# Performance work log

Measured on AMD Instinct MI355X. Metric: run time of the kernel, lower is better.

## Reference

```python
import jax, jax.numpy as jnp
import numpy as np

B, N, D = 2, 2048, 256
H = 8
HD = D // H
SCALE = HD ** 0.5  # NOTE: source MULTIPLIES by sqrt(head_dim)
EPS = 1e-5
DFF = 4 * D


def setup_inputs() -> dict:
    key = jax.random.key(0)
    ks = jax.random.split(key, 9)
    s = lambda fan_in: 1.0 / np.sqrt(fan_in)
    return {
        "x": jax.random.normal(ks[0], (B, N, D), dtype=jnp.float32),
        # weights stored [in, out] (transposed torch Linear)
        "qkv_w": jax.random.normal(ks[1], (D, 3 * D), dtype=jnp.float32) * s(D),
        "proj_w": jax.random.normal(ks[2], (D, D), dtype=jnp.float32) * s(D),
        "proj_b": jax.random.normal(ks[3], (D,), dtype=jnp.float32) * 0.01,
        "fc1_w": jax.random.normal(ks[4], (D, DFF), dtype=jnp.float32) * s(D),
        "fc1_b": jax.random.normal(ks[5], (DFF,), dtype=jnp.float32) * 0.01,
        "fc2_w": jax.random.normal(ks[6], (DFF, D), dtype=jnp.float32) * s(DFF),
        "fc2_b": jax.random.normal(ks[7], (D,), dtype=jnp.float32) * 0.01,
        "ln1_g": jnp.ones((D,), dtype=jnp.float32),
        "ln1_b": jnp.zeros((D,), dtype=jnp.float32),
    }


def _layernorm(x, g, b):
    mu = jnp.mean(x, axis=-1, keepdims=True)
    var = jnp.mean(jnp.square(x - mu), axis=-1, keepdims=True)
    return (x - mu) * jax.lax.rsqrt(var + EPS) * g + b


def reference(x, qkv_w, proj_w, proj_b, fc1_w, fc1_b, fc2_w, fc2_b, ln1_g, ln1_b):
    b, n, d = x.shape
    # --- MHA ---
    qkv = (x @ qkv_w).reshape(b, n, 3, H, HD)
    q = qkv[:, :, 0].transpose(0, 2, 1, 3)  # [B,H,N,HD]
    k = qkv[:, :, 1].transpose(0, 2, 1, 3)
    v = qkv[:, :, 2].transpose(0, 2, 1, 3)
    att = jnp.einsum("bhqd,bhkd->bhqk", q, k) * SCALE  # multiplied, per source
    att = jax.nn.softmax(att, axis=-1)
    out = jnp.einsum("bhqk,bhkd->bhqd", att, v)
    out = out.transpose(0, 2, 1, 3).reshape(b, n, d)
    out = out @ proj_w + proj_b
    # --- post-norm residual ---
    net = _layernorm(out + x, ln1_g, ln1_b)
    shortcut = net
    # --- MLP (NO activation in source forward) ---
    net = (net @ fc1_w + fc1_b) @ fc2_w + fc2_b
    return net + shortcut
```

## Files before the change

kernel.cpp:

```cpp
#include <hip/hip_runtime.h>


typedef __attribute__((ext_vector_type(8))) short short8;
typedef __attribute__((ext_vector_type(4))) short short4v;
typedef __attribute__((ext_vector_type(8))) _Float16 half8;
typedef __attribute__((ext_vector_type(4))) _Float16 half4;
typedef __attribute__((ext_vector_type(2))) __fp16 fp16x2;
typedef __attribute__((ext_vector_type(4))) float floatx4;
typedef __attribute__((ext_vector_type(2))) unsigned int uint2v;
typedef unsigned short u16;

#define MFMAG(a,b,c)  __builtin_amdgcn_mfma_f32_16x16x32_f16((a),(b),(c),0,0,0)
#if __has_builtin(__builtin_amdgcn_mfma_f32_16x16x16_f16)
#define MFMAPV(a,b,c) __builtin_amdgcn_mfma_f32_16x16x16_f16((a),(b),(c),0,0,0)
#else
#define MFMAPV(a,b,c) __builtin_amdgcn_mfma_f32_16x16x16f16((a),(b),(c),0,0,0)
#endif
#define CLF 8.1615404f

#if __has_builtin(__builtin_amdgcn_exp2f)
#define EX2(x) __builtin_amdgcn_exp2f(x)
#else
#define EX2(x) exp2f(x)
#endif

__device__ __forceinline__ float bf2f(u16 u) { return __uint_as_float(((unsigned)u) << 16); }
__device__ __forceinline__ float h2f(u16 u) { _Float16 h = *(_Float16*)&u; return (float)h; }
__device__ __forceinline__ u16 f2h(float f) { _Float16 h = (_Float16)f; return *(u16*)&h; }
__device__ __forceinline__ unsigned pkh2(float a, float b) {
#if __has_builtin(__builtin_amdgcn_cvt_pkrtz)
  fp16x2 h = __builtin_amdgcn_cvt_pkrtz(a, b);
  return *(unsigned*)&h;
#else
  return (unsigned)f2h(a) | ((unsigned)f2h(b) << 16);
#endif
}
__device__ __forceinline__ void gll16(const void* g, void* l) {
  __builtin_amdgcn_global_load_lds((const __attribute__((address_space(1))) void*)g,
                                   (__attribute__((address_space(3))) void*)l, 16, 0, 0);
}

__global__ __launch_bounds__(256) void prep_k(
    const void* __restrict__ x, const void* __restrict__ qkv_w,
    const void* __restrict__ proj_w, const void* __restrict__ fc1_w,
    const void* __restrict__ fc2_w, const void* __restrict__ proj_b,
    const void* __restrict__ fc1_b, const void* __restrict__ fc2_b,
    const void* __restrict__ ln_g, const void* __restrict__ ln_b,
    u16* __restrict__ x_f, u16* __restrict__ wq_f,
    u16* __restrict__ wt_proj, u16* __restrict__ wt_fc1, u16* __restrict__ wt_fc2,
    u16* __restrict__ b_proj, u16* __restrict__ b_fc1, u16* __restrict__ b_fc2,
    u16* __restrict__ g_ln, u16* __restrict__ bb_ln)
{
  __shared__ u16 tr[64][70];
  const int lane = threadIdx.x & 63;
  const float probe = bf2f(((const u16*)qkv_w)[lane]);
  const bool f32 = __ballot(!(fabsf(probe) < 1000.0f)) != 0ull;
  const int bid = blockIdx.x, tid = threadIdx.x;
  #define RD(p, i) (f32 ? ((const float*)(p))[i] : bf2f(((const u16*)(p))[i]))
  if (bid < 1024) {
    const size_t i = (size_t)bid * 1024 + tid * 4;
    const u16 o0 = f2h(RD(x, i)),     o1 = f2h(RD(x, i + 1));
    const u16 o2 = f2h(RD(x, i + 2)), o3 = f2h(RD(x, i + 3));
    short4v sv = {(short)o0, (short)o1, (short)o2, (short)o3};
    *(short4v*)&x_f[i] = sv;
  } else if (bid < 1216) {
    int idx = bid - 1024;
    const void* src; u16* dst; int Ns, Kt, tk, tn;
    if (idx < 48)       { src = qkv_w;  dst = wq_f;    Ns = 768;  Kt = 256;
                          tk = idx & 3;  tn = idx >> 2; }
    else if (idx < 64)  { idx -= 48;  src = proj_w; dst = wt_proj; Ns = 256; Kt = 256;
                          tk = idx & 3;  tn = idx >> 2; }
    else if (idx < 128) { idx -= 64;  src = fc1_w;  dst = wt_fc1;  Ns = 1024; Kt = 256;
                          tk = idx & 3;  tn = idx >> 2; }
    else                { idx -= 128; src = fc2_w;  dst = wt_fc2;  Ns = 256;  Kt = 1024;
                          tk = idx & 15; tn = idx >> 4; }
    const int k0 = tk * 64, n0 = tn * 64;
    const int r = tid >> 6, c = tid & 63;
#pragma unroll
    for (int p = 0; p < 16; ++p) {
      const int k = k0 + p * 4 + r;
      tr[c][p * 4 + r] = f2h(RD(src, (size_t)k * Ns + n0 + c));
    }
    __syncthreads();
#pragma unroll
    for (int p = 0; p < 16; ++p) {
      const int n = n0 + p * 4 + r;
      dst[(size_t)n * Kt + k0 + c] = tr[p * 4 + r][c];
    }
  } else {
    const int j = (bid - 1216) * 256 + tid;
    if (j < 256)       b_proj[j]        = f2h(RD(proj_b, j));
    else if (j < 1280) b_fc1[j - 256]   = f2h(RD(fc1_b, j - 256));
    else if (j < 1536) b_fc2[j - 1280]  = f2h(RD(fc2_b, j - 1280));
    else if (j < 1792) g_ln[j - 1536]   = f2h(RD(ln_g, j - 1536));
    else if (j < 2048) bb_ln[j - 1792]  = f2h(RD(ln_b, j - 1792));
  }
  #undef RD
}

template<int TW, int EPI, bool BIAS, bool RES, bool COMB>
__global__ __launch_bounds__(256) void gemm_k(
    const u16* __restrict__ A, const u16* __restrict__ Bt, const u16* __restrict__ A2,
    const u16* __restrict__ bias, const u16* __restrict__ res,
    void* __restrict__ out0, u16* __restrict__ aux1, u16* __restrict__ aux3,
    const float* __restrict__ muc,
    int M, int Nn, int K)
{
  constexpr int BT = TW * 32;
  constexpr int NC = TW / 2;
  __shared__ __align__(16) u16 As[BT][40];
  __shared__ __align__(16) u16 Bs[BT][40];
  __shared__ __align__(16) u16 Vt[(EPI == 2) ? 64 * 72 : 1];
  const int tid = threadIdx.x;
  const int m0 = blockIdx.y * BT, n0 = blockIdx.x * BT;
  const int wid = tid >> 6, lane = tid & 63;
  const int wm = (wid >> 1) * (TW * 16), wn = (wid & 1) * (TW * 16);
  const int lm = lane & 15, quad = lane >> 4;

  floatx4 zero = {0.f, 0.f, 0.f, 0.f};
  floatx4 acc[TW][TW];
#pragma unroll
  for (int i = 0; i < TW; ++i)
#pragma unroll
    for (int j = 0; j < TW; ++j) acc[i][j] = zero;

  auto comb8 = [&](int t, int col8) -> short8 {
    const size_t o = (size_t)t * 256 + col8;
    const int h = col8 >> 5;
    const float m0_ = muc[t * 8 + h],          m1_ = muc[32768 + t * 8 + h];
    const float m2_ = muc[65536 + t * 8 + h],  m3_ = muc[98304 + t * 8 + h];
    const float M = fmaxf(fmaxf(m0_, m1_), fmaxf(m2_, m3_));
    float w0 = EX2(m0_ - M), w1 = EX2(m1_ - M), w2 = EX2(m2_ - M), w3 = EX2(m3_ - M);
    const float inv = 1.f / (w0 + w1 + w2 + w3);
    w0 *= inv; w1 *= inv; w2 *= inv; w3 *= inv;
    short8 a0 = *(const short8*)&A[o],  a1 = *(const short8*)&A[o + 1048576];
    short8 a2 = *(const short8*)&A2[o], a3 = *(const short8*)&A2[o + 1048576];
    float v[8];
#pragma unroll
    for (int j = 0; j < 8; ++j)
      v[j] = w0 * h2f((u16)a0[j]) + w1 * h2f((u16)a1[j])
           + w2 * h2f((u16)a2[j]) + w3 * h2f((u16)a3[j]);
    uint2v uu0 = {pkh2(v[0], v[1]), pkh2(v[2], v[3])};
    uint2v uu1 = {pkh2(v[4], v[5]), pkh2(v[6], v[7])};
    short8 r;
    *(uint2v*)&r = uu0; *((uint2v*)&r + 1) = uu1;
    return r;
  };

  int srow[NC], soff[NC];
#pragma unroll
  for (int c = 0; c < NC; ++c) {
    const int cid = tid * NC + c;
    srow[c] = cid >> 2; soff[c] = (cid & 3) * 8;
  }

  short8 ra0[NC], rb0[NC];
  auto ld = [&](int kk) {
#pragma unroll
    for (int c = 0; c < NC; ++c) {
      rb0[c] = *(const short8*)&Bt[(size_t)(n0 + srow[c]) * K + kk + soff[c]];
      if (COMB) ra0[c] = comb8(m0 + srow[c], kk + soff[c]);
      else      ra0[c] = *(const short8*)&A[(size_t)(m0 + srow[c]) * K + kk + soff[c]];
    }
  };
  ld(0);
  for (int k0 = 0; k0 < K; k0 += 32) {
    if (k0) __syncthreads();
#pragma unroll
    for (int c = 0; c < NC; ++c) {
      *(short8*)&As[srow[c]][soff[c]] = ra0[c];
      *(short8*)&Bs[srow[c]][soff[c]] = rb0[c];
    }
    __syncthreads();
    if (k0 + 32 < K) ld(k0 + 32);
    half8 fa[TW], fb[TW];
#pragma unroll
    for (int t = 0; t < TW; ++t) {
      fa[t] = *(const half8*)&As[wm + t * 16 + lm][quad * 8];
      fb[t] = *(const half8*)&Bs[wn + t * 16 + lm][quad * 8];
    }
#pragma unroll
    for (int i = 0; i < TW; ++i)
#pragma unroll
      for (int j = 0; j < TW; ++j)
        acc[i][j] = MFMAG(fa[i], fb[j], acc[i][j]);
  }

  if (EPI == 2 && n0 >= 512) {
    __syncthreads();
#pragma unroll
    for (int i = 0; i < TW; ++i)
#pragma unroll
      for (int j = 0; j < TW; ++j)
#pragma unroll
        for (int r = 0; r < 4; ++r)
          Vt[(wn + j * 16 + lm) * 72 + wm + i * 16 + quad * 4 + r] = f2h(acc[i][j][r]);
    __syncthreads();
    const int bb = m0 >> 11, n = m0 & 2047;
#pragma unroll
    for (int pass = 0; pass < 2; ++pass) {
      const int dl = (tid >> 3) + pass * 32;
      const int oct = tid & 7;
      const int col = n0 - 512 + dl;
      const int d = col & 31, hh = col >> 5;
      short8 v = *(const short8*)&Vt[dl * 72 + oct * 8];
      *(short8*)&((u16*)out0)[(size_t)((bb * 8 + hh) * 32 + d) * 2048 + n + oct * 8] = v;
    }
    return;
  }

#pragma unroll
  for (int i = 0; i < TW; ++i) {
    const int rowb = m0 + wm + i * 16 + quad * 4;
#pragma unroll
    for (int j = 0; j < TW; ++j) {
      const int col = n0 + wn + j * 16 + lm;
      const float bv = BIAS ? h2f(bias[col]) : 0.f;
#pragma unroll
      for (int r = 0; r < 4; ++r) {
        const int row = rowb + r;
        float v = acc[i][j][r] + bv;
        const size_t o = (size_t)row * Nn + col;
        if (RES) v += h2f(res[o]);
        if (EPI == 0) {
          ((float*)out0)[o] = v;
        } else if (EPI == 1) {
          ((u16*)out0)[o] = f2h(v);
        } else {
          if (col < 256) aux1[(size_t)row * 256 + col] = f2h(v);
          else           aux3[(size_t)row * 256 + (col - 256)] = f2h(v);
        }
      }
    }
  }
}

__global__ __launch_bounds__(512) void gemm8_k(
    const u16* __restrict__ A, const u16* __restrict__ Bt,
    const u16* __restrict__ bias, const u16* __restrict__ res,
    float* __restrict__ out0, int Nn, int K)
{
  __shared__ __align__(16) u16 As[64][40];
  __shared__ __align__(16) u16 Bs[64][40];
  const int tid = threadIdx.x;
  const int m0 = blockIdx.y * 64, n0 = blockIdx.x * 64;
  const int wid = tid >> 6, lane = tid & 63;
  const int wm = (wid & 3) * 16, wn = (wid >> 2) * 32;
  const int lm = lane & 15, quad = lane >> 4;

  floatx4 zero = {0.f, 0.f, 0.f, 0.f};
  floatx4 acc0 = zero, acc1 = zero;

  const int sgrp = tid >> 8, stid = tid & 255;
  const int srow = stid >> 2, soff = (stid & 3) * 8;
  const u16* sp = sgrp ? Bt : A;
  const int sbase = sgrp ? n0 : m0;

  short8 rr;
  rr = *(const short8*)&sp[(size_t)(sbase + srow) * K + soff];
  for (int k0 = 0; k0 < K; k0 += 32) {
    if (k0) __syncthreads();
    if (sgrp) *(short8*)&Bs[srow][soff] = rr;
    else      *(short8*)&As[srow][soff] = rr;
    __syncthreads();
    if (k0 + 32 < K)
      rr = *(const short8*)&sp[(size_t)(sbase + srow) * K + k0 + 32 + soff];
    half8 fa = *(const half8*)&As[wm + lm][quad * 8];
    half8 fb0 = *(const half8*)&Bs[wn + lm][quad * 8];
    half8 fb1 = *(const half8*)&Bs[wn + 16 + lm][quad * 8];
    acc0 = MFMAG(fa, fb0, acc0);
    acc1 = MFMAG(fa, fb1, acc1);
  }

  const int rowb = m0 + wm + quad * 4;
  const int col0 = n0 + wn + lm, col1 = col0 + 16;
  const float bv0 = h2f(bias[col0]), bv1 = h2f(bias[col1]);
#pragma unroll
  for (int r = 0; r < 4; ++r) {
    const int row = rowb + r;
    const size_t o0 = (size_t)row * Nn + col0;
    const size_t o1 = (size_t)row * Nn + col1;
    out0[o0] = acc0[r] + bv0 + h2f(res[o0]);
    out0[o1] = acc1[r] + bv1 + h2f(res[o1]);
  }
}

__global__ __launch_bounds__(512) void projln8_k(
    const u16* __restrict__ A,
    const u16* __restrict__ A2,
    const u16* __restrict__ Bt,
    const u16* __restrict__ bias,
    const u16* xh,
    const u16* __restrict__ g, const u16* __restrict__ bb,
    const float* __restrict__ muc,
    u16* net)
{
  __shared__ __align__(16) u16 As[16][40];
  __shared__ __align__(16) u16 Bs[256][40];
  __shared__ float ss[8][16], ssq[8][16];
  const int tid = threadIdx.x;
  const int m0 = blockIdx.x * 16;
  const int wid = tid >> 6, lane = tid & 63;
  const int lm = lane & 15, quad = lane >> 4;

  floatx4 zero = {0.f, 0.f, 0.f, 0.f};
  floatx4 acc0 = zero, acc1 = zero;

  auto comb8 = [&](int t, int col8) -> short8 {
    const size_t o = (size_t)t * 256 + col8;
    const int h = col8 >> 5;
    const float m0_ = muc[t * 8 + h],          m1_ = muc[32768 + t * 8 + h];
    const float m2_ = muc[65536 + t * 8 + h],  m3_ = muc[98304 + t * 8 + h];
    const float M = fmaxf(fmaxf(m0_, m1_), fmaxf(m2_, m3_));
    float w0 = EX2(m0_ - M), w1 = EX2(m1_ - M), w2 = EX2(m2_ - M), w3 = EX2(m3_ - M);
    const float inv = 1.f / (w0 + w1 + w2 + w3);
    w0 *= inv; w1 *= inv; w2 *= inv; w3 *= inv;
    short8 a0 = *(const short8*)&A[o],  a1 = *(const short8*)&A[o + 1048576];
    short8 a2 = *(const short8*)&A2[o], a3 = *(const short8*)&A2[o + 1048576];
    float v[8];
#pragma unroll
    for (int j = 0; j < 8; ++j)
      v[j] = w0 * h2f((u16)a0[j]) + w1 * h2f((u16)a1[j])
           + w2 * h2f((u16)a2[j]) + w3 * h2f((u16)a3[j]);
    uint2v uu0 = {pkh2(v[0], v[1]), pkh2(v[2], v[3])};
    uint2v uu1 = {pkh2(v[4], v[5]), pkh2(v[6], v[7])};
    short8 r;
    *(uint2v*)&r = uu0; *((uint2v*)&r + 1) = uu1;
    return r;
  };

  const int arow = lane >> 2, aoff = (lane & 3) * 8;
  int brow0 = wid * 32 + (lane >> 2), brow1 = brow0 + 16;
  const int boff = (lane & 3) * 8;

  short8 ra, rb0, rb1;
  if (wid == 0) ra = comb8(m0 + arow, aoff);
  rb0 = *(const short8*)&Bt[(size_t)brow0 * 256 + boff];
  rb1 = *(const short8*)&Bt[(size_t)brow1 * 256 + boff];

  for (int k0 = 0; k0 < 256; k0 += 32) {
    if (k0) __syncthreads();
    if (wid == 0) *(short8*)&As[arow][aoff] = ra;
    *(short8*)&Bs[brow0][boff] = rb0;
    *(short8*)&Bs[brow1][boff] = rb1;
    __syncthreads();
    if (k0 + 32 < 256) {
      if (wid == 0) ra = comb8(m0 + arow, k0 + 32 + aoff);
      rb0 = *(const short8*)&Bt[(size_t)brow0 * 256 + k0 + 32 + boff];
      rb1 = *(const short8*)&Bt[(size_t)brow1 * 256 + k0 + 32 + boff];
    }
    half8 fa = *(const half8*)&As[lm][quad * 8];
    half8 fb0 = *(const half8*)&Bs[wid * 32 + lm][quad * 8];
    half8 fb1 = *(const half8*)&Bs[wid * 32 + 16 + lm][quad * 8];
    acc0 = MFMAG(fa, fb0, acc0);
    acc1 = MFMAG(fa, fb1, acc1);
  }

  const int col0 = wid * 32 + lm, col1 = col0 + 16;
  const float bv0 = h2f(bias[col0]), bv1 = h2f(bias[col1]);
  float s[4], sq[4], v0[4], v1[4];
#pragma unroll
  for (int r = 0; r < 4; ++r) {
    const int row = quad * 4 + r;
    const float a = acc0[r] + bv0 + h2f(xh[(size_t)(m0 + row) * 256 + col0]);
    const float b = acc1[r] + bv1 + h2f(xh[(size_t)(m0 + row) * 256 + col1]);
    v0[r] = a; v1[r] = b;
    s[r] = a + b; sq[r] = a * a + b * b;
  }
#pragma unroll
  for (int d = 1; d < 16; d <<= 1)
#pragma unroll
    for (int r = 0; r < 4; ++r) {
      s[r] += __shfl_xor(s[r], d);
      sq[r] += __shfl_xor(sq[r], d);
    }
  if (lm == 0)
#pragma unroll
    for (int r = 0; r < 4; ++r) { ss[wid][quad * 4 + r] = s[r]; ssq[wid][quad * 4 + r] = sq[r]; }
  __syncthreads();
#pragma unroll
  for (int r = 0; r < 4; ++r) {
    const int row = quad * 4 + r;
    float ts = 0.f, tq = 0.f;
#pragma unroll
    for (int w = 0; w < 8; ++w) { ts += ss[w][row]; tq += ssq[w][row]; }
    const float mean = ts * (1.f / 256.f);
    const float var = tq * (1.f / 256.f) - mean * mean;
    const float is = rsqrtf(var + 1e-5f);
    net[(size_t)(m0 + row) * 256 + col0] =
        f2h((v0[r] - mean) * is * h2f(g[col0]) + h2f(bb[col0]));
    net[(size_t)(m0 + row) * 256 + col1] =
        f2h((v1[r] - mean) * is * h2f(g[col1]) + h2f(bb[col1]));
  }
}

template<int CHUNKS>
__global__ __launch_bounds__(256) void attn_k(
    const u16* __restrict__ qf16, const u16* __restrict__ kf16,
    const u16* __restrict__ vt, u16* __restrict__ outp, u16* __restrict__ out23,
    float* __restrict__ mu)
{
  __shared__ __align__(16) u16 Ks[2][64][32];
  __shared__ __align__(16) u16 Vs[2][32][64];
  const int tid = threadIdx.x, wid = tid >> 6, lane = tid & 63;
  const int lm = lane & 15, quad = lane >> 4;
  const int bid = blockIdx.x;
  const int chunk = (CHUNKS > 1) ? (bid >> 9) : 0;
  const int qblk = bid & 31, bh = (bid >> 5) & 15;
  const int b = bh >> 3, h = bh & 7;
  const int q0 = qblk * 64 + wid * 16;
  const size_t tb = (size_t)b * 2048;
  const int NT = 32 / CHUNKS;
  const int kofs = chunk * (2048 / CHUNKS);

  half8 qh;
  { size_t off = (tb + q0 + lm) * 256 + h * 32 + quad * 8;
    qh = *(const half8*)&qf16[off]; }

  const int kkey = tid >> 2, kg = tid & 3;
  const size_t kb = (tb + kofs + kkey) * 256 + h * 32 + kg * 8;
  const int vd = tid >> 3, vp = tid & 7, vk8 = vp ^ (vd & 7);
  const size_t vb = (size_t)(bh * 32 + vd) * 2048 + kofs + vk8 * 8;

  gll16(kf16 + kb, (u16*)Ks + tid * 8);
  gll16(vt  + vb,  (u16*)Vs + tid * 8);

  float mrun = -1e30f, lrun = 0.f;
  floatx4 o0 = {0.f,0.f,0.f,0.f}, o1 = {0.f,0.f,0.f,0.f};

  for (int kt = 0; kt < NT; ++kt) {
    const int buf = kt & 1;
    __syncthreads();
    if (kt < NT - 1) {
      const int nb = (buf ^ 1) * 2048;
      const size_t ko = (size_t)(kt + 1) * 16384;
      const size_t vo = (size_t)(kt + 1) * 64;
      gll16(kf16 + kb + ko, (u16*)Ks + nb + tid * 8);
      gll16(vt  + vb + vo,  (u16*)Vs + nb + tid * 8);
    }

    floatx4 z[4];
#pragma unroll
    for (int kf = 0; kf < 4; ++kf) {
      half8 khf = *(const half8*)&Ks[buf][kf * 16 + lm][quad * 8];
      floatx4 zz = {0.f,0.f,0.f,0.f};
      z[kf] = MFMAG(khf, qh, zz);
    }
    float zm = fmaxf(fmaxf(fmaxf(z[0][0], z[0][1]), fmaxf(z[0][2], z[0][3])),
               fmaxf(fmaxf(z[1][0], z[1][1]), fmaxf(z[1][2], z[1][3])));
    zm = fmaxf(zm, fmaxf(fmaxf(fmaxf(z[2][0], z[2][1]), fmaxf(z[2][2], z[2][3])),
                   fmaxf(fmaxf(z[3][0], z[3][1]), fmaxf(z[3][2], z[3][3]))));
    zm = fmaxf(zm, __shfl_xor(zm, 16));
    zm = fmaxf(zm, __shfl_xor(zm, 32));
    const float mn = fmaxf(mrun, zm);
    const float alpha = EX2((mrun - mn) * CLF);
    const float mc = mn * CLF;
    mrun = mn;
    float ls = 0.f;
    half4 pb[4];
#pragma unroll
    for (int kf = 0; kf < 4; ++kf) {
      const float p0 = EX2(__builtin_fmaf(z[kf][0], CLF, -mc));
      const float p1 = EX2(__builtin_fmaf(z[kf][1], CLF, -mc));
      const float p2 = EX2(__builtin_fmaf(z[kf][2], CLF, -mc));
      const float p3 = EX2(__builtin_fmaf(z[kf][3], CLF, -mc));
      ls += (p0 + p1) + (p2 + p3);
      uint2v uu = {pkh2(p0, p1), pkh2(p2, p3)};
      pb[kf] = *(half4*)&uu;
    }
    ls += __shfl_xor(ls, 16);
    ls += __shfl_xor(ls, 32);
    lrun = lrun * alpha + ls;
#pragma unroll
    for (int r = 0; r < 4; ++r) { o0[r] *= alpha; o1[r] *= alpha; }
    const u16* vbase = (const u16*)Vs + buf * 2048;
#pragma unroll
    for (int kf = 0; kf < 4; ++kf) {
      const int k8 = 2 * kf + (quad >> 1);
      const int d0 = lm, d1 = 16 + lm;
      half4 vf0 = *(const half4*)(vbase + (d0 * 8 + (k8 ^ (d0 & 7))) * 8 + (quad & 1) * 4);
      half4 vf1 = *(const half4*)(vbase + (d1 * 8 + (k8 ^ (d1 & 7))) * 8 + (quad & 1) * 4);
      o0 = MFMAPV(vf0, pb[kf], o0);
      o1 = MFMAPV(vf1, pb[kf], o1);
    }
  }
  const float inv = 1.0f / lrun;
  const size_t tok = tb + q0 + lm;
  u16* dst = ((CHUNKS > 2 && chunk >= 2) ? out23 : outp) + (size_t)(chunk & 1) * 1048576;
  const size_t rowo = tok * 256 + h * 32;
#pragma unroll
  for (int r = 0; r < 4; ++r) {
    dst[rowo + quad * 4 + r]      = f2h(o0[r] * inv);
    dst[rowo + 16 + quad * 4 + r] = f2h(o1[r] * inv);
  }
  if (CHUNKS > 1 && quad == 0)
    mu[chunk * 32768 + tok * 8 + h] = __builtin_fmaf(mrun, CLF, __log2f(lrun));
}

template<int CHUNKS>
__global__ __launch_bounds__(256) void combine_k(u16* __restrict__ d,
                                                 const u16* __restrict__ e,
                                                 const float* __restrict__ mu)
{
  const int t = blockIdx.x, c = threadIdx.x, h = c >> 5;
  const size_t o = (size_t)t * 256 + c;
  float m[CHUNKS];
  float M = -1e30f;
#pragma unroll
  for (int i = 0; i < CHUNKS; ++i) { m[i] = mu[i * 32768 + t * 8 + h]; M = fmaxf(M, m[i]); }
  float wsum = 0.f, acc = 0.f;
#pragma unroll
  for (int i = 0; i < CHUNKS; ++i) {
    const float w = EX2(m[i] - M);
    const u16 v = (i < 2) ? d[o + (size_t)i * 1048576] : e[o + (size_t)(i - 2) * 1048576];
    wsum += w; acc += w * h2f(v);
  }
  d[o] = f2h(acc / wsum);
}

__global__ __launch_bounds__(256) void ln_k(const float* __restrict__ pf,
                                            const u16* __restrict__ xh,
                                            const u16* __restrict__ g,
                                            const u16* __restrict__ bta,
                                            u16* __restrict__ net)
{
  const int t = blockIdx.x, c = threadIdx.x;
  const size_t o = (size_t)t * 256 + c;
  float v = pf[o] + h2f(xh[o]);
  float s = v, s2 = v * v;
#pragma unroll
  for (int d = 1; d < 64; d <<= 1) { s += __shfl_xor(s, d); s2 += __shfl_xor(s2, d); }
  __shared__ float ss[4], ss2[4];
  const int w = c >> 6;
  if ((c & 63) == 0) { ss[w] = s; ss2[w] = s2; }
  __syncthreads();
  s = ss[0] + ss[1] + ss[2] + ss[3];
  s2 = ss2[0] + ss2[1] + ss2[2] + ss2[3];
  const float mu = s * (1.f / 256.f);
  const float var = s2 * (1.f / 256.f) - mu * mu;
  const float is = rsqrtf(var + 1e-5f);
  net[o] = f2h((v - mu) * is * h2f(g[c]) + h2f(bta[c]));
}

extern "C" void kernel_launch(void* const* d_in, const int* in_sizes, int n_in,
                              void* d_out, int out_size, void* d_ws, size_t ws_size,
                              hipStream_t stream) {
  const void* x      = d_in[0];
  const void* qkv_w  = d_in[1];
  const void* proj_w = d_in[2];
  const void* proj_b = d_in[3];
  const void* fc1_w  = d_in[4];
  const void* fc1_b  = d_in[5];
  const void* fc2_w  = d_in[6];
  const void* fc2_b  = d_in[7];
  const void* ln_g   = d_in[8];
  const void* ln_b   = d_in[9];

  char* ws = (char*)d_ws;
  u16* b_proj  = (u16*)(ws + 4096);
  u16* b_fc1   = (u16*)(ws + 8192);
  u16* b_fc2   = (u16*)(ws + 12288);
  u16* g_ln    = (u16*)(ws + 16384);
  u16* bb_ln   = (u16*)(ws + 20480);
  u16* wq_f    = (u16*)(ws + 131072);
  u16* wt_proj = (u16*)(ws + 524288);
  u16* wt_fc1  = (u16*)(ws + 655360);
  u16* wt_fc2  = (u16*)(ws + 1179648);
  u16* x_f     = (u16*)(ws + 2097152);
  u16* q_f16   = (u16*)(ws + 4194304);
  u16* k_f16   = (u16*)(ws + 6291456);
  u16* vt      = (u16*)(ws + 8388608);
  float* mu    = (float*)(ws + 10485760);
  u16* out23   = (u16*)(ws + 11010048);
  u16* attn    = (u16*)d_out;

  u16* net4    = x_f;
  u16* hbuf4   = (u16*)(ws + 4194304);

  float* projf = (float*)(ws + 4194304);
  u16* net     = (u16*)(ws + 11010048);
  u16* hbuf    = (u16*)(ws + 2097152);

  const bool sk4 = ws_size >= 15204352;
  const bool sk2 = ws_size >= 11010048;

  prep_k<<<1224, 256, 0, stream>>>(x, qkv_w, proj_w, fc1_w, fc2_w,
                                   proj_b, fc1_b, fc2_b, ln_g, ln_b,
                                   x_f, wq_f, wt_proj, wt_fc1, wt_fc2,
                                   b_proj, b_fc1, b_fc2, g_ln, bb_ln);

  gemm_k<2, 2, false, false, false><<<dim3(12, 64), 256, 0, stream>>>(
      x_f, wq_f, nullptr, nullptr, nullptr, vt, q_f16, k_f16, nullptr, 4096, 768, 256);
  if (sk4) {
    attn_k<4><<<2048, 256, 0, stream>>>(q_f16, k_f16, vt, attn, out23, mu);
    projln8_k<<<256, 512, 0, stream>>>(attn, out23, wt_proj, b_proj, x_f,
                                       g_ln, bb_ln, mu, net4);
    gemm_k<2, 1, true, false, false><<<dim3(16, 64), 256, 0, stream>>>(
        net4, wt_fc1, nullptr, b_fc1, nullptr, hbuf4, nullptr, nullptr, nullptr,
        4096, 1024, 256);
    gemm8_k<<<dim3(4, 64), 512, 0, stream>>>(
        hbuf4, wt_fc2, b_fc2, net4, (float*)d_out, 256, 1024);
    return;
  }
  if (sk2) {
    attn_k<2><<<1024, 256, 0, stream>>>(q_f16, k_f16, vt, attn, nullptr, mu);
    combine_k<2><<<4096, 256, 0, stream>>>(attn, nullptr, mu);
    gemm_k<2, 0, true, false, false><<<dim3(4, 64), 256, 0, stream>>>(
        attn, wt_proj, nullptr, b_proj, nullptr, projf, nullptr, nullptr, nullptr,
        4096, 256, 256);
  } else {
    attn_k<1><<<512, 256, 0, stream>>>(q_f16, k_f16, vt, attn, nullptr, nullptr);
    gemm_k<2, 0, true, false, false><<<dim3(4, 64), 256, 0, stream>>>(
        attn, wt_proj, nullptr, b_proj, nullptr, projf, nullptr, nullptr, nullptr,
        4096, 256, 256);
  }
  ln_k<<<4096, 256, 0, stream>>>(projf, x_f, g_ln, bb_ln, net);
  gemm_k<2, 1, true, false, false><<<dim3(16, 64), 256, 0, stream>>>(
      net, wt_fc1, nullptr, b_fc1, nullptr, hbuf, nullptr, nullptr, nullptr,
      4096, 1024, 256);
  gemm_k<2, 0, true, true, false><<<dim3(4, 64), 256, 0, stream>>>(
      hbuf, wt_fc2, nullptr, b_fc2, net, d_out, nullptr, nullptr, nullptr,
      4096, 256, 1024);
}
```

Baseline: 144.5 us.

## Fuse input/weight conversion into QKV GEMM kernel and read raw x in proj-LN

Adds a qkvprep_k kernel that loads raw x and qkv_w directly, converts them to fp16 on the fly and computes the QKV GEMM. Extra blocks in the same launch transpose and convert the remaining weights and biases. This removes the separate prep kernel launch and the round trip of writing and rereading converted x and qkv weights. projln8_k now reads the raw input for the residual, so x_f is no longer needed. The cost is strided, uncoalesced loads of qkv_w inside the GEMM and repeated conversion work in every block.

```diff
diff --git a/kernel.cpp b/kernel.cpp
--- a/kernel.cpp
+++ b/kernel.cpp
@@ -38,6 +38,159 @@
 __device__ __forceinline__ void gll16(const void* g, void* l) {
   __builtin_amdgcn_global_load_lds((const __attribute__((address_space(1))) void*)g,
                                    (__attribute__((address_space(3))) void*)l, 16, 0, 0);
+}
+
+__global__ __launch_bounds__(256) void qkvprep_k(
+    const void* __restrict__ x, const void* __restrict__ qkv_w,
+    const void* __restrict__ proj_w, const void* __restrict__ fc1_w,
+    const void* __restrict__ fc2_w, const void* __restrict__ proj_b,
+    const void* __restrict__ fc1_b, const void* __restrict__ fc2_b,
+    const void* __restrict__ ln_g, const void* __restrict__ ln_b,
+    u16* __restrict__ wt_proj, u16* __restrict__ wt_fc1, u16* __restrict__ wt_fc2,
+    u16* __restrict__ b_proj, u16* __restrict__ b_fc1, u16* __restrict__ b_fc2,
+    u16* __restrict__ g_ln, u16* __restrict__ bb_ln,
+    u16* __restrict__ vt, u16* __restrict__ qf, u16* __restrict__ kf)
+{
+  __shared__ __align__(16) u16 lds[9728];
+  const int tid = threadIdx.x;
+  const int lane = tid & 63;
+  const float probe = bf2f(((const u16*)qkv_w)[lane]);
+  const bool f32 = __ballot(!(fabsf(probe) < 1000.0f)) != 0ull;
+  const int bid = blockIdx.x;
+  #define RD(p, i) (f32 ? ((const float*)(p))[i] : bf2f(((const u16*)(p))[i]))
+
+  if (bid >= 768) {
+    int idx = bid - 768;
+    if (idx < 144) {
+      u16 (*tr)[70] = (u16(*)[70])lds;
+      const void* src; u16* dst; int Ns, Kt, tk, tn;
+      if (idx < 16)      { src = proj_w; dst = wt_proj; Ns = 256;  Kt = 256;
+                           tk = idx & 3;  tn = idx >> 2; }
+      else if (idx < 80) { idx -= 16; src = fc1_w; dst = wt_fc1; Ns = 1024; Kt = 256;
+                           tk = idx & 3;  tn = idx >> 2; }
+      else               { idx -= 80; src = fc2_w; dst = wt_fc2; Ns = 256;  Kt = 1024;
+                           tk = idx & 15; tn = idx >> 4; }
+      const int k0 = tk * 64, n0v = tn * 64;
+      const int r = tid >> 6, c = tid & 63;
+#pragma unroll
+      for (int p = 0; p < 16; ++p) {
+        const int k = k0 + p * 4 + r;
+        tr[c][p * 4 + r] = f2h(RD(src, (size_t)k * Ns + n0v + c));
+      }
+      __syncthreads();
+#pragma unroll
+      for (int p = 0; p < 16; ++p) {
+        const int n = n0v + p * 4 + r;
+        dst[(size_t)n * Kt + k0 + c] = tr[p * 4 + r][c];
+      }
+    } else {
+      const int j = (idx - 144) * 256 + tid;
+      if (j < 256)       b_proj[j]        = f2h(RD(proj_b, j));
+      else if (j < 1280) b_fc1[j - 256]   = f2h(RD(fc1_b, j - 256));
+      else if (j < 1536) b_fc2[j - 1280]  = f2h(RD(fc2_b, j - 1280));
+      else if (j < 1792) g_ln[j - 1536]   = f2h(RD(ln_g, j - 1536));
+      else if (j < 2048) bb_ln[j - 1792]  = f2h(RD(ln_b, j - 1792));
+    }
+    return;
+  }
+  #undef RD
+
+  u16 (*As)[40] = (u16(*)[40])lds;
+  u16 (*Bs)[40] = (u16(*)[40])(lds + 2560);
+  u16* Vt = lds + 5120;
+  const int mb = bid / 12, nb = bid % 12;
+  const int m0 = mb * 64, n0 = nb * 64;
+  const int wid = tid >> 6;
+  const int wm = (wid >> 1) * 32, wn = (wid & 1) * 32;
+  const int lm = lane & 15, quad = lane >> 4;
+
+  floatx4 zero = {0.f, 0.f, 0.f, 0.f};
+  floatx4 acc[2][2] = {{zero, zero}, {zero, zero}};
+
+  const int arow = tid >> 2, aoff = (tid & 3) * 8;
+  const int bn = tid & 63, bk8 = (tid >> 6) * 8;
+
+  short8 rah, rbh;
+  auto ld = [&](int kk) {
+    if (f32) {
+      const float* xp = (const float*)x + (size_t)(m0 + arow) * 256 + kk + aoff;
+      floatx4 a0 = *(const floatx4*)xp;
+      floatx4 a1 = *(const floatx4*)(xp + 4);
+#pragma unroll
+      for (int j = 0; j < 4; ++j) {
+        rah[j]     = (short)f2h(a0[j]);
+        rah[4 + j] = (short)f2h(a1[j]);
+      }
+      const float* wp = (const float*)qkv_w + (size_t)(kk + bk8) * 768 + n0 + bn;
+#pragma unroll
+      for (int j = 0; j < 8; ++j) rbh[j] = (short)f2h(wp[(size_t)j * 768]);
+    } else {
+      short8 a = *(const short8*)((const u16*)x + (size_t)(m0 + arow) * 256 + kk + aoff);
+#pragma unroll
+      for (int j = 0; j < 8; ++j) rah[j] = (short)f2h(bf2f((u16)a[j]));
+      const u16* wp = (const u16*)qkv_w + (size_t)(kk + bk8) * 768 + n0 + bn;
+#pragma unroll
+      for (int j = 0; j < 8; ++j) rbh[j] = (short)f2h(bf2f(wp[(size_t)j * 768]));
+    }
+  };
+  ld(0);
+  for (int k0 = 0; k0 < 256; k0 += 32) {
+    if (k0) __syncthreads();
+    *(short8*)&As[arow][aoff] = rah;
+    *(short8*)&Bs[bn][bk8] = rbh;
+    __syncthreads();
+    if (k0 + 32 < 256) ld(k0 + 32);
+    half8 fa[2], fb[2];
+#pragma unroll
+    for (int t = 0; t < 2; ++t) {
+      fa[t] = *(const half8*)&As[wm + t * 16 + lm][quad * 8];
+      fb[t] = *(const half8*)&Bs[wn + t * 16 + lm][quad * 8];
+    }
+#pragma unroll
+    for (int i = 0; i < 2; ++i)
+#pragma unroll
+      for (int j = 0; j < 2; ++j)
+        acc[i][j] = MFMAG(fa[i], fb[j], acc[i][j]);
+  }
+
+  if (n0 >= 512) {
+    __syncthreads();
+#pragma unroll
+    for (int i = 0; i < 2; ++i)
+#pragma unroll
+      for (int j = 0; j < 2; ++j)
+#pragma unroll
+        for (int r = 0; r < 4; ++r)
+          Vt[(wn + j * 16 + lm) * 72 + wm + i * 16 + quad * 4 + r] = f2h(acc[i][j][r]);
+    __syncthreads();
+    const int bb = m0 >> 11, n = m0 & 2047;
+#pragma unroll
+    for (int pass = 0; pass < 2; ++pass) {
+      const int dl = (tid >> 3) + pass * 32;
+      const int oct = tid & 7;
+      const int col = n0 - 512 + dl;
+      const int d = col & 31, hh = col >> 5;
+      short8 v = *(const short8*)&Vt[dl * 72 + oct * 8];
+      *(short8*)&vt[(size_t)((bb * 8 + hh) * 32 + d) * 2048 + n + oct * 8] = v;
+    }
+    return;
+  }
+
+#pragma unroll
+  for (int i = 0; i < 2; ++i) {
+    const int rowb = m0 + wm + i * 16 + quad * 4;
+#pragma unroll
+    for (int j = 0; j < 2; ++j) {
+      const int col = n0 + wn + j * 16 + lm;
+#pragma unroll
+      for (int r = 0; r < 4; ++r) {
+        const int row = rowb + r;
+        const u16 hv = f2h(acc[i][j][r]);
+        if (col < 256) qf[(size_t)row * 256 + col] = hv;
+        else           kf[(size_t)row * 256 + (col - 256)] = hv;
+      }
+    }
+  }
 }
 
 __global__ __launch_bounds__(256) void prep_k(
@@ -290,10 +443,11 @@
     const u16* __restrict__ A2,
     const u16* __restrict__ Bt,
     const u16* __restrict__ bias,
-    const u16* xh,
+    const void* __restrict__ xraw,
+    const void* __restrict__ probew,
     const u16* __restrict__ g, const u16* __restrict__ bb,
     const float* __restrict__ muc,
-    u16* net)
+    u16* __restrict__ net)
 {
   __shared__ __align__(16) u16 As[16][40];
   __shared__ __align__(16) u16 Bs[256][40];
@@ -302,6 +456,8 @@
   const int m0 = blockIdx.x * 16;
   const int wid = tid >> 6, lane = tid & 63;
   const int lm = lane & 15, quad = lane >> 4;
+  const float probe = bf2f(((const u16*)probew)[lane]);
+  const bool f32 = __ballot(!(fabsf(probe) < 1000.0f)) != 0ull;
 
   floatx4 zero = {0.f, 0.f, 0.f, 0.f};
   floatx4 acc0 = zero, acc1 = zero;
@@ -362,8 +518,12 @@
 #pragma unroll
   for (int r = 0; r < 4; ++r) {
     const int row = quad * 4 + r;
-    const float a = acc0[r] + bv0 + h2f(xh[(size_t)(m0 + row) * 256 + col0]);
-    const float b = acc1[r] + bv1 + h2f(xh[(size_t)(m0 + row) * 256 + col1]);
+    const size_t o0 = (size_t)(m0 + row) * 256 + col0;
+    const size_t o1 = (size_t)(m0 + row) * 256 + col1;
+    const float x0 = f32 ? ((const float*)xraw)[o0] : bf2f(((const u16*)xraw)[o0]);
+    const float x1 = f32 ? ((const float*)xraw)[o1] : bf2f(((const u16*)xraw)[o1]);
+    const float a = acc0[r] + bv0 + h2f(f2h(x0));
+    const float b = acc1[r] + bv1 + h2f(f2h(x1));
     v0[r] = a; v1[r] = b;
     s[r] = a + b; sq[r] = a * a + b * b;
   }
@@ -574,7 +734,7 @@
   u16* out23   = (u16*)(ws + 11010048);
   u16* attn    = (u16*)d_out;
 
-  u16* net4    = x_f;
+  u16* net4    = (u16*)(ws + 2097152);
   u16* hbuf4   = (u16*)(ws + 4194304);
 
   float* projf = (float*)(ws + 4194304);
@@ -584,16 +744,14 @@
   const bool sk4 = ws_size >= 15204352;
   const bool sk2 = ws_size >= 11010048;
 
-  prep_k<<<1224, 256, 0, stream>>>(x, qkv_w, proj_w, fc1_w, fc2_w,
-                                   proj_b, fc1_b, fc2_b, ln_g, ln_b,
-                                   x_f, wq_f, wt_proj, wt_fc1, wt_fc2,
-                                   b_proj, b_fc1, b_fc2, g_ln, bb_ln);
-
-  gemm_k<2, 2, false, false, false><<<dim3(12, 64), 256, 0, stream>>>(
-      x_f, wq_f, nullptr, nullptr, nullptr, vt, q_f16, k_f16, nullptr, 4096, 768, 256);
   if (sk4) {
+    qkvprep_k<<<920, 256, 0, stream>>>(x, qkv_w, proj_w, fc1_w, fc2_w,
+                                       proj_b, fc1_b, fc2_b, ln_g, ln_b,
+                                       wt_proj, wt_fc1, wt_fc2,
+                                       b_proj, b_fc1, b_fc2, g_ln, bb_ln,
+                                       vt, q_f16, k_f16);
     attn_k<4><<<2048, 256, 0, stream>>>(q_f16, k_f16, vt, attn, out23, mu);
-    projln8_k<<<256, 512, 0, stream>>>(attn, out23, wt_proj, b_proj, x_f,
+    projln8_k<<<256, 512, 0, stream>>>(attn, out23, wt_proj, b_proj, x, qkv_w,
                                        g_ln, bb_ln, mu, net4);
     gemm_k<2, 1, true, false, false><<<dim3(16, 64), 256, 0, stream>>>(
         net4, wt_fc1, nullptr, b_fc1, nullptr, hbuf4, nullptr, nullptr, nullptr,
@@ -602,6 +760,13 @@
         hbuf4, wt_fc2, b_fc2, net4, (float*)d_out, 256, 1024);
     return;
   }
+
+  prep_k<<<1224, 256, 0, stream>>>(x, qkv_w, proj_w, fc1_w, fc2_w,
+                                   proj_b, fc1_b, fc2_b, ln_g, ln_b,
+                                   x_f, wq_f, wt_proj, wt_fc1, wt_fc2,
+                                   b_proj, b_fc1, b_fc2, g_ln, bb_ln);
+  gemm_k<2, 2, false, false, false><<<dim3(12, 64), 256, 0, stream>>>(
+      x_f, wq_f, nullptr, nullptr, nullptr, vt, q_f16, k_f16, nullptr, 4096, 768, 256);
   if (sk2) {
     attn_k<2><<<1024, 256, 0, stream>>>(q_f16, k_f16, vt, attn, nullptr, mu);
     combine_k<2><<<4096, 256, 0, stream>>>(attn, nullptr, mu);
```

Result: faster. 141.2 us (-2.3%).
